# Performance work log

Measured on AMD Instinct MI355X. Metric: run time of the kernel, lower is better.

## Reference

```python
import jax, jax.numpy as jnp
import numpy as np

USER_NUM = 100000
ITEM_NUM = 50000
N_NODES = USER_NUM + ITEM_NUM
EMB = 64
N_LAYERS = 3
N_EDGES = 4000000


def setup_inputs() -> dict:
    key = jax.random.key(0)
    k1, k2, k3, k4, k5 = jax.random.split(key, 5)
    user_emb = jax.random.normal(k1, (USER_NUM, EMB), dtype=jnp.float32)
    item_emb = jax.random.normal(k2, (ITEM_NUM, EMB), dtype=jnp.float32)
    # COO sparse normalized adjacency (values would be 1/sqrt(deg_u*deg_v) in the real graph)
    edge_vals = jax.random.uniform(k3, (N_EDGES,), dtype=jnp.float32)
    edge_src = jax.random.randint(k4, (N_EDGES,), 0, N_NODES, dtype=jnp.int32)
    edge_dst = jax.random.randint(k5, (N_EDGES,), 0, N_NODES, dtype=jnp.int32)
    return {"user_emb": user_emb, "item_emb": item_emb, "edge_vals": edge_vals,
            "edge_src": edge_src, "edge_dst": edge_dst}


def reference(user_emb, item_emb, edge_vals, edge_src, edge_dst):
    # emb = cat([user_emb, item_emb])  -> [N, d]
    emb = jnp.concatenate([user_emb, item_emb], axis=0)
    acc = emb  # running sum over layer embeddings (fuses stack+mean)
    for _ in range(N_LAYERS):
        # SpMM: (A @ emb) via gather -> scale -> segment scatter-add
        msg = edge_vals[:, None] * emb[edge_src]          # [E, d]
        emb = jax.ops.segment_sum(msg, edge_dst, num_segments=N_NODES)
        acc = acc + emb
    final_emb = acc / jnp.float32(N_LAYERS + 1)            # mean over L+1 layer embeddings
    # original returns (final_emb[:user_num], final_emb[user_num:], all_emb);
    # user/item split is a trivial slice of this single array
    return final_emb
```

## Files before the change

kernel.cpp:

```cpp
#include <hip/hip_runtime.h>
#include <hip/hip_fp16.h>

constexpr int USER_NUM = 100000;
constexpr int ITEM_NUM = 50000;
constexpr int N_NODES  = USER_NUM + ITEM_NUM;
constexpr int EMB      = 64;
constexpr int N_LAYERS = 3;
constexpr int NB       = (N_NODES + 511) >> 9;
constexpr int TILE     = 2048;
constexpr int CAP      = 16368;


__device__ inline unsigned pack_f16_2(float a, float b) {
    __half2 h = __floats2half2_rn(a, b);
    return __builtin_bit_cast(unsigned, h);
}

__device__ inline float2 unp_f16_2(unsigned u) {
    return __half22float2(__builtin_bit_cast(__half2, u));
}

__device__ inline void hfma4(uint4 u, __half2 v, __half2* a) {
    a[0] = __hfma2(__builtin_bit_cast(__half2, u.x), v, a[0]);
    a[1] = __hfma2(__builtin_bit_cast(__half2, u.y), v, a[1]);
    a[2] = __hfma2(__builtin_bit_cast(__half2, u.z), v, a[2]);
    a[3] = __hfma2(__builtin_bit_cast(__half2, u.w), v, a[3]);
}


__global__ __launch_bounds__(256) void init_f16_k(const float4* __restrict__ user,
                                                  const float4* __restrict__ item,
                                                  uint4* __restrict__ embA,
                                                  int total8, int user8) {
    int g = blockIdx.x * 256 + threadIdx.x;
    if (g >= total8) return;
    const float4* s4;
    int base;
    if (g < user8) { s4 = user; base = g * 2; }
    else           { s4 = item; base = (g - user8) * 2; }
    float4 lo = s4[base];
    float4 hi = s4[base + 1];
    uint4 o;
    o.x = pack_f16_2(lo.x, lo.y);
    o.y = pack_f16_2(lo.z, lo.w);
    o.z = pack_f16_2(hi.x, hi.y);
    o.w = pack_f16_2(hi.z, hi.w);
    embA[g] = o;
}


__global__ __launch_bounds__(256) void partition_k(const float* __restrict__ vals,
                                                   const int* __restrict__ src,
                                                   const int* __restrict__ dst,
                                                   int* __restrict__ gcursor,
                                                   unsigned* __restrict__ rkey,
                                                   unsigned short* __restrict__ rvalq,
                                                   int n_edges) {
    __shared__ int lhist[NB];
    __shared__ int loff[NB];
    __shared__ int lcur[NB];
    __shared__ int gb[NB];
    __shared__ unsigned long long stage[TILE];

    int tid = threadIdx.x;
    int base = blockIdx.x * TILE;
    int n = min(TILE, n_edges - base);

    for (int b = tid; b < NB; b += 256) lhist[b] = 0;
    __syncthreads();

    unsigned key[8];
    unsigned short vq[8];
    short bk[8];
    #pragma unroll
    for (int j = 0; j < 8; ++j) {
        int k = j * 256 + tid;
        if (k < n) {
            int e = base + k;
            int d = dst[e];
            int b = d >> 9;
            key[j] = (unsigned)src[e] | ((unsigned)(d & 511) << 18);
            vq[j]  = (unsigned short)min((unsigned)(vals[e] * 16384.0f + 0.5f), 16383u);
            bk[j]  = (short)b;
            atomicAdd(&lhist[b], 1);
        } else bk[j] = -1;
    }
    __syncthreads();

    for (int b = tid; b < NB; b += 256) {
        int c = lhist[b];
        if (c > 0) gb[b] = atomicAdd(&gcursor[b], c);
    }

    if (tid < 64) {
        int carry = 0;
        #pragma unroll
        for (int c = 0; c < (NB + 63) / 64; ++c) {
            int idx = c * 64 + tid;
            int v = (idx < NB) ? lhist[idx] : 0;
            int x = v;
            #pragma unroll
            for (int off = 1; off < 64; off <<= 1) {
                int y = __shfl_up(x, off);
                if (tid >= off) x += y;
            }
            if (idx < NB) { loff[idx] = carry + x - v; lcur[idx] = carry + x - v; }
            carry += __shfl(x, 63);
        }
    }
    __syncthreads();

    #pragma unroll
    for (int j = 0; j < 8; ++j) {
        if (bk[j] >= 0) {
            int slot = atomicAdd(&lcur[bk[j]], 1);
            stage[slot] = (unsigned long long)key[j]
                        | ((unsigned long long)vq[j] << 27)
                        | ((unsigned long long)(unsigned)bk[j] << 41);
        }
    }
    __syncthreads();

    for (int slot = tid; slot < n; slot += 256) {
        unsigned long long rec = stage[slot];
        int b = (int)(rec >> 41);
        int pos = gb[b] + (slot - loff[b]);
        if (pos < CAP) {
            size_t idx = (size_t)b * CAP + pos;
            rkey[idx]  = (unsigned)(rec & 0x7FFFFFFu);
            rvalq[idx] = (unsigned short)((rec >> 27) & 0x3FFFu);
        }
    }
}

__global__ __launch_bounds__(1024) void csrfin_k(const int* __restrict__ gcursor,
                                                 const unsigned* __restrict__ rkey,
                                                 const unsigned short* __restrict__ rvalq,
                                                 unsigned* __restrict__ pairs,
                                                 int* __restrict__ rowbeg,
                                                 int* __restrict__ rowend) {
    __shared__ int lhist[512];
    __shared__ int lcur[512];
    __shared__ int wsum[8];
    int b = blockIdx.x;
    int node_base = b << 9;
    int nn = min(512, N_NODES - node_base);
    int tid = threadIdx.x;
    int cnt = min(gcursor[b], CAP);
    int rbase = b * CAP;

    if (tid < 512) lhist[tid] = 0;
    __syncthreads();
    for (int i = tid; i < cnt; i += 1024)
        atomicAdd(&lhist[rkey[rbase + i] >> 18], 1);
    __syncthreads();

    if (tid < 512) {
        int lane = tid & 63, wid = tid >> 6;
        int v = lhist[tid];
        int x = v;
        #pragma unroll
        for (int off = 1; off < 64; off <<= 1) {
            int y = __shfl_up(x, off);
            if (lane >= off) x += y;
        }
        if (lane == 63) wsum[wid] = x;
        __syncthreads();
        if (tid == 0) {
            int c = 0;
            #pragma unroll
            for (int j = 0; j < 8; ++j) { int t = wsum[j]; wsum[j] = c; c += t; }
        }
        __syncthreads();
        int excl = wsum[wid] + x - v;
        if (tid < nn) {
            rowbeg[node_base + tid] = rbase + excl;
            rowend[node_base + tid] = rbase + excl + v;
            lcur[tid] = rbase + excl;
        }
    } else {
        __syncthreads();
        __syncthreads();
    }
    __syncthreads();

    for (int i = tid; i < cnt; i += 1024) {
        unsigned k = rkey[rbase + i];
        unsigned valq = rvalq[rbase + i];
        int local = (int)(k >> 18);
        unsigned s = k & 0x3FFFFu;
        int pos = atomicAdd(&lcur[local], 1);
        pairs[pos] = s | (valq << 18);
    }
}


template <int LAST>
__global__ __launch_bounds__(256) void gather_k(const int* __restrict__ rowbeg,
                                                const int* __restrict__ rowend,
                                                const unsigned* __restrict__ pairs,
                                                const uint4* __restrict__ emb,
                                                uint4* __restrict__ nxt,
                                                float4* __restrict__ outf,
                                                const uint4* __restrict__ e1,
                                                const uint4* __restrict__ e2,
                                                const float4* __restrict__ user,
                                                const float4* __restrict__ item) {
    int wid  = threadIdx.x >> 6;
    int node = blockIdx.x * 4 + wid;
    if (node >= N_NODES) return;
    int lane = threadIdx.x & 63;
    int sub  = lane >> 3;
    int q    = lane & 7;

    int beg = rowbeg[node];
    int end = rowend[node];

    __half2 h0[4], h1[4], h2[4], h3[4];
    #pragma unroll
    for (int j = 0; j < 4; ++j) {
        h0[j] = __float2half2_rn(0.0f);
        h1[j] = __float2half2_rn(0.0f);
        h2[j] = __float2half2_rn(0.0f);
        h3[j] = __float2half2_rn(0.0f);
    }

    const float kInv = 1.0f / 16384.0f;
    for (int p = beg; p < end; p += 32) {
        int i0 = p + sub, i1 = p + 8 + sub, i2 = p + 16 + sub, i3 = p + 24 + sub;
        unsigned u0 = (i0 < end) ? pairs[i0] : 0u;
        unsigned u1 = (i1 < end) ? pairs[i1] : 0u;
        unsigned u2 = (i2 < end) ? pairs[i2] : 0u;
        unsigned u3 = (i3 < end) ? pairs[i3] : 0u;
        uint4 x0 = emb[(size_t)(u0 & 0x3FFFFu) * 8 + q];
        uint4 x1 = emb[(size_t)(u1 & 0x3FFFFu) * 8 + q];
        uint4 x2 = emb[(size_t)(u2 & 0x3FFFFu) * 8 + q];
        uint4 x3 = emb[(size_t)(u3 & 0x3FFFFu) * 8 + q];
        hfma4(x0, __float2half2_rn((float)(u0 >> 18) * kInv), h0);
        hfma4(x1, __float2half2_rn((float)(u1 >> 18) * kInv), h1);
        hfma4(x2, __float2half2_rn((float)(u2 >> 18) * kInv), h2);
        hfma4(x3, __float2half2_rn((float)(u3 >> 18) * kInv), h3);
    }

    float s[8];
    #pragma unroll
    for (int j = 0; j < 4; ++j) {
        float2 f0 = __half22float2(h0[j]);
        float2 f1 = __half22float2(h1[j]);
        float2 f2 = __half22float2(h2[j]);
        float2 f3 = __half22float2(h3[j]);
        s[2 * j]     = (f0.x + f1.x) + (f2.x + f3.x);
        s[2 * j + 1] = (f0.y + f1.y) + (f2.y + f3.y);
    }
    #pragma unroll
    for (int j = 0; j < 8; ++j) {
        float t = s[j];
        t += __shfl_xor(t, 8);
        t += __shfl_xor(t, 16);
        t += __shfl_xor(t, 32);
        s[j] = t;
    }

    if (sub == 0) {
        if (LAST) {
            int fb = node * 16 + q * 2;
            float4 u0 = (node < USER_NUM) ? user[fb]     : item[(node - USER_NUM) * 16 + q * 2];
            float4 u1 = (node < USER_NUM) ? user[fb + 1] : item[(node - USER_NUM) * 16 + q * 2 + 1];
            uint4 b1 = e1[(size_t)node * 8 + q];
            uint4 b2 = e2[(size_t)node * 8 + q];
            float2 a1[4], a2[4];
            a1[0] = unp_f16_2(b1.x); a1[1] = unp_f16_2(b1.y);
            a1[2] = unp_f16_2(b1.z); a1[3] = unp_f16_2(b1.w);
            a2[0] = unp_f16_2(b2.x); a2[1] = unp_f16_2(b2.y);
            a2[2] = unp_f16_2(b2.z); a2[3] = unp_f16_2(b2.w);
            float4 r0, r1;
            r0.x = (u0.x + a1[0].x + a2[0].x + s[0]) * 0.25f;
            r0.y = (u0.y + a1[0].y + a2[0].y + s[1]) * 0.25f;
            r0.z = (u0.z + a1[1].x + a2[1].x + s[2]) * 0.25f;
            r0.w = (u0.w + a1[1].y + a2[1].y + s[3]) * 0.25f;
            r1.x = (u1.x + a1[2].x + a2[2].x + s[4]) * 0.25f;
            r1.y = (u1.y + a1[2].y + a2[2].y + s[5]) * 0.25f;
            r1.z = (u1.z + a1[3].x + a2[3].x + s[6]) * 0.25f;
            r1.w = (u1.w + a1[3].y + a2[3].y + s[7]) * 0.25f;
            outf[fb]     = r0;
            outf[fb + 1] = r1;
        } else {
            uint4 o;
            o.x = pack_f16_2(s[0], s[1]);
            o.y = pack_f16_2(s[2], s[3]);
            o.z = pack_f16_2(s[4], s[5]);
            o.w = pack_f16_2(s[6], s[7]);
            nxt[(size_t)node * 8 + q] = o;
        }
    }
}


__global__ __launch_bounds__(256) void fb_init_k(const float4* __restrict__ user,
                                                 const float4* __restrict__ item,
                                                 float4* __restrict__ embA,
                                                 float4* __restrict__ acc,
                                                 int total4, int user4) {
    int i = blockIdx.x * 256 + threadIdx.x;
    if (i >= total4) return;
    float4 v = (i < user4) ? user[i] : item[i - user4];
    embA[i] = v;
    acc[i]  = v;
}

__global__ __launch_bounds__(256) void scatter_k(const float* __restrict__ emb,
                                                 const float* __restrict__ vals,
                                                 const int*   __restrict__ src,
                                                 const int*   __restrict__ dst,
                                                 float* __restrict__ out,
                                                 int n_edges) {
    long long gtid = (long long)blockIdx.x * 256 + threadIdx.x;
    int e = (int)(gtid >> 4);
    if (e >= n_edges) return;
    int lane = (int)(gtid & 15);
    float v = vals[e];
    float4 x = ((const float4*)(emb + (size_t)src[e] * EMB))[lane];
    float* o = out + (size_t)dst[e] * EMB + (size_t)lane * 4;
    unsafeAtomicAdd(o + 0, v * x.x);
    unsafeAtomicAdd(o + 1, v * x.y);
    unsafeAtomicAdd(o + 2, v * x.z);
    unsafeAtomicAdd(o + 3, v * x.w);
}

__global__ __launch_bounds__(256) void acc_k(float4* __restrict__ acc,
                                             const float4* __restrict__ emb, int total4) {
    int i = blockIdx.x * 256 + threadIdx.x;
    if (i >= total4) return;
    float4 a = acc[i], b = emb[i];
    a.x += b.x; a.y += b.y; a.z += b.z; a.w += b.w;
    acc[i] = a;
}

__global__ __launch_bounds__(256) void scale_k(float4* __restrict__ acc, float s, int total4) {
    int i = blockIdx.x * 256 + threadIdx.x;
    if (i >= total4) return;
    float4 a = acc[i];
    a.x *= s; a.y *= s; a.z *= s; a.w *= s;
    acc[i] = a;
}

extern "C" void kernel_launch(void* const* d_in, const int* in_sizes, int n_in,
                              void* d_out, int out_size, void* d_ws, size_t ws_size,
                              hipStream_t stream) {
    const float* user = (const float*)d_in[0];
    const float* item = (const float*)d_in[1];
    const float* vals = (const float*)d_in[2];
    const int*   src  = (const int*)d_in[3];
    const int*   dst  = (const int*)d_in[4];
    float* out = (float*)d_out;

    const int n_edges = in_sizes[2];
    const size_t embf32_bytes = (size_t)N_NODES * EMB * sizeof(float);
    const size_t embf16_bytes = (size_t)N_NODES * EMB * 2;

    const int total4 = N_NODES * EMB / 4;
    const int user4  = USER_NUM * EMB / 4;
    const int total8 = N_NODES * EMB / 8;
    const int user8  = USER_NUM * EMB / 8;
    const int blocks_e4 = (total4 + 255) / 256;
    const int blocks_e8 = (total8 + 255) / 256;

    size_t off = 0;
    uint4*    bufA  = (uint4*)((char*)d_ws + off); off += embf16_bytes;
    uint4*    bufB  = (uint4*)((char*)d_ws + off); off += embf16_bytes;
    uint4*    bufC  = (uint4*)((char*)d_ws + off); off += embf16_bytes;
    unsigned* pairs = (unsigned*)((char*)d_ws + off); off += (size_t)NB * CAP * sizeof(unsigned);
    int*      rowbeg= (int*)((char*)d_ws + off); off += (size_t)N_NODES * sizeof(int);
    int*      rowend= (int*)((char*)d_ws + off); off += (size_t)N_NODES * sizeof(int);
    int*      gcursor=(int*)((char*)d_ws + off); off += (size_t)NB * sizeof(int);

    unsigned*       rkey  = (unsigned*)bufB;
    unsigned short* rvalq = (unsigned short*)bufC;

    if (ws_size < off || n_edges >= (1 << 22)) {
        float* fA = (float*)d_ws;
        float* fB = (float*)((char*)d_ws + embf32_bytes);
        fb_init_k<<<blocks_e4, 256, 0, stream>>>((const float4*)user, (const float4*)item,
                                                 (float4*)fA, (float4*)out, total4, user4);
        const long long work = (long long)n_edges * 16;
        const int blocks_s = (int)((work + 255) / 256);
        float* cur = fA; float* nxt = fB;
        for (int l = 0; l < N_LAYERS; ++l) {
            hipMemsetAsync(nxt, 0, embf32_bytes, stream);
            scatter_k<<<blocks_s, 256, 0, stream>>>(cur, vals, src, dst, nxt, n_edges);
            acc_k<<<blocks_e4, 256, 0, stream>>>((float4*)out, (const float4*)nxt, total4);
            float* t = cur; cur = nxt; nxt = t;
        }
        scale_k<<<blocks_e4, 256, 0, stream>>>((float4*)out, 1.0f / (N_LAYERS + 1), total4);
        return;
    }

    const int blocks_p = (n_edges + TILE - 1) / TILE;
    hipMemsetAsync(gcursor, 0, (size_t)NB * sizeof(int), stream);
    partition_k<<<blocks_p, 256, 0, stream>>>(vals, src, dst, gcursor, rkey, rvalq, n_edges);
    csrfin_k<<<NB, 1024, 0, stream>>>(gcursor, rkey, rvalq, pairs, rowbeg, rowend);

    init_f16_k<<<blocks_e8, 256, 0, stream>>>((const float4*)user, (const float4*)item,
                                              bufA, total8, user8);

    const int blocks_g = (N_NODES + 3) / 4;
    gather_k<0><<<blocks_g, 256, 0, stream>>>(rowbeg, rowend, pairs, bufA, bufB, nullptr,
                                              nullptr, nullptr, nullptr, nullptr);
    gather_k<0><<<blocks_g, 256, 0, stream>>>(rowbeg, rowend, pairs, bufB, bufC, nullptr,
                                              nullptr, nullptr, nullptr, nullptr);
    gather_k<1><<<blocks_g, 256, 0, stream>>>(rowbeg, rowend, pairs, bufC, nullptr, (float4*)out,
                                              bufB, bufC,
                                              (const float4*)user, (const float4*)item);
}
```

Baseline: 341.5 us.

## Pad CSR rows to 4 entries, vectorize pair loads, store values as fp16 bits

```diff
diff --git a/kernel.cpp b/kernel.cpp
--- a/kernel.cpp
+++ b/kernel.cpp
@@ -25,6 +25,11 @@
     a[1] = __hfma2(__builtin_bit_cast(__half2, u.y), v, a[1]);
     a[2] = __hfma2(__builtin_bit_cast(__half2, u.z), v, a[2]);
     a[3] = __hfma2(__builtin_bit_cast(__half2, u.w), v, a[3]);
+}
+
+__device__ inline __half2 dec_val(unsigned u) {
+    unsigned b = u >> 18;
+    return __builtin_bit_cast(__half2, (b << 16) | b);
 }
 
 
@@ -80,7 +85,8 @@
             int d = dst[e];
             int b = d >> 9;
             key[j] = (unsigned)src[e] | ((unsigned)(d & 511) << 18);
-            vq[j]  = (unsigned short)min((unsigned)(vals[e] * 16384.0f + 0.5f), 16383u);
+            unsigned hb = (unsigned)__half_as_ushort(__float2half_rn(vals[e]));
+            vq[j]  = (unsigned short)min(hb, 0x3FFFu);
             bk[j]  = (short)b;
             atomicAdd(&lhist[b], 1);
         } else bk[j] = -1;
@@ -157,8 +163,9 @@
 
     if (tid < 512) {
         int lane = tid & 63, wid = tid >> 6;
-        int v = lhist[tid];
-        int x = v;
+        int v  = lhist[tid];
+        int p4 = (v + 3) & ~3;
+        int x = p4;
         #pragma unroll
         for (int off = 1; off < 64; off <<= 1) {
             int y = __shfl_up(x, off);
@@ -172,11 +179,13 @@
             for (int j = 0; j < 8; ++j) { int t = wsum[j]; wsum[j] = c; c += t; }
         }
         __syncthreads();
-        int excl = wsum[wid] + x - v;
+        int excl = wsum[wid] + x - p4;
         if (tid < nn) {
-            rowbeg[node_base + tid] = rbase + excl;
-            rowend[node_base + tid] = rbase + excl + v;
-            lcur[tid] = rbase + excl;
+            int beg = rbase + excl;
+            int end = min(beg + v, rbase + CAP);
+            rowbeg[node_base + tid] = beg;
+            rowend[node_base + tid] = end;
+            lcur[tid] = beg;
         }
     } else {
         __syncthreads();
@@ -184,13 +193,14 @@
     }
     __syncthreads();
 
+    int cap_end = rbase + CAP;
     for (int i = tid; i < cnt; i += 1024) {
         unsigned k = rkey[rbase + i];
         unsigned valq = rvalq[rbase + i];
         int local = (int)(k >> 18);
         unsigned s = k & 0x3FFFFu;
         int pos = atomicAdd(&lcur[local], 1);
-        pairs[pos] = s | (valq << 18);
+        if (pos < cap_end) pairs[pos] = s | (valq << 18);
     }
 }
 
@@ -225,21 +235,21 @@
         h3[j] = __float2half2_rn(0.0f);
     }
 
-    const float kInv = 1.0f / 16384.0f;
     for (int p = beg; p < end; p += 32) {
-        int i0 = p + sub, i1 = p + 8 + sub, i2 = p + 16 + sub, i3 = p + 24 + sub;
-        unsigned u0 = (i0 < end) ? pairs[i0] : 0u;
-        unsigned u1 = (i1 < end) ? pairs[i1] : 0u;
-        unsigned u2 = (i2 < end) ? pairs[i2] : 0u;
-        unsigned u3 = (i3 < end) ? pairs[i3] : 0u;
+        int i = p + sub * 4;
+        uint4 u4 = *reinterpret_cast<const uint4*>(pairs + i);
+        unsigned u0 = (i + 0 < end) ? u4.x : 0u;
+        unsigned u1 = (i + 1 < end) ? u4.y : 0u;
+        unsigned u2 = (i + 2 < end) ? u4.z : 0u;
+        unsigned u3 = (i + 3 < end) ? u4.w : 0u;
         uint4 x0 = emb[(size_t)(u0 & 0x3FFFFu) * 8 + q];
         uint4 x1 = emb[(size_t)(u1 & 0x3FFFFu) * 8 + q];
         uint4 x2 = emb[(size_t)(u2 & 0x3FFFFu) * 8 + q];
         uint4 x3 = emb[(size_t)(u3 & 0x3FFFFu) * 8 + q];
-        hfma4(x0, __float2half2_rn((float)(u0 >> 18) * kInv), h0);
-        hfma4(x1, __float2half2_rn((float)(u1 >> 18) * kInv), h1);
-        hfma4(x2, __float2half2_rn((float)(u2 >> 18) * kInv), h2);
-        hfma4(x3, __float2half2_rn((float)(u3 >> 18) * kInv), h3);
+        hfma4(x0, dec_val(u0), h0);
+        hfma4(x1, dec_val(u1), h1);
+        hfma4(x2, dec_val(u2), h2);
+        hfma4(x3, dec_val(u3), h3);
     }
 
     float s[8];
```

Result: no change. 347.0 us (+1.6%).
